# Performance work log

Hardware: AMD Instinct MI355X
Metric: run time of the kernel (lower is better)

Reference implementation:

```python
import jax, jax.numpy as jnp
import numpy as np

B, D, U1, U2 = 16384, 512, 512, 512
BN_EPS = 1e-3  # keras BatchNormalization default epsilon


def sparsemax(z):
    # z: [..., D]; standard sparsemax along last axis (Martins & Astudillo)
    d = z.shape[-1]
    z_sorted = -jnp.sort(-z, axis=-1)                      # descending
    z_cum = jnp.cumsum(z_sorted, axis=-1)
    k = jnp.arange(1, d + 1, dtype=z.dtype)
    support = (1.0 + k * z_sorted) > z_cum                 # [..., D] bool
    k_z = jnp.sum(support, axis=-1, keepdims=True)         # support size
    tau = (jnp.take_along_axis(z_cum, k_z.astype(jnp.int32) - 1, axis=-1) - 1.0) / k_z.astype(z.dtype)
    return jnp.maximum(z - tau, 0.0)


def setup_inputs() -> dict:
    key = jax.random.key(0)
    ks = jax.random.split(key, 8)
    x = jax.random.normal(ks[0], (B, D), dtype=jnp.float32)
    W1 = jax.random.normal(ks[1], (D, U1), dtype=jnp.float32) * 0.05
    b1 = jnp.zeros((U1,), jnp.float32)
    centers = jax.random.normal(ks[2], (U2, D), dtype=jnp.float32)      # paraboloid centers
    coefs = jax.random.normal(ks[3], (U2, D), dtype=jnp.float32) * 0.1  # paraboloid axis coefficients
    bn_gamma = jnp.ones((D,), jnp.float32)
    bn_beta = jnp.zeros((D,), jnp.float32)
    bn_mean = jnp.zeros((D,), jnp.float32)
    bn_var = jnp.ones((D,), jnp.float32)
    W_out = jax.random.normal(ks[4], (U1 + U2, D), dtype=jnp.float32) * 0.05
    b_out = jnp.zeros((D,), jnp.float32)
    w_add = jnp.array([0.5, 0.5], jnp.float32)  # WeightedAdd learnable scalars
    return {"x": x, "W1": W1, "b1": b1, "centers": centers, "coefs": coefs,
            "bn_gamma": bn_gamma, "bn_beta": bn_beta, "bn_mean": bn_mean, "bn_var": bn_var,
            "W_out": W_out, "b_out": b_out, "w_add": w_add}


def reference(x, W1, b1, centers, coefs, bn_gamma, bn_beta, bn_mean, bn_var, W_out, b_out, w_add):
    # Dense branch
    h1 = jax.nn.relu(x @ W1 + b1)                               # [B, U1]
    # BoundedParaboloids branch: BatchNorm (inference stats) then bounded paraboloids
    xb = (x - bn_mean) * jax.lax.rsqrt(bn_var + BN_EPS) * bn_gamma + bn_beta
    # q_j = sum_d (coefs[j,d] * (xb_d - centers[j,d]))^2, computed via GEMMs
    A = coefs * coefs                                            # [U2, D]
    q = (xb * xb) @ A.T - 2.0 * (xb @ (A * centers).T) + jnp.sum(A * centers * centers, axis=-1)
    h2 = jax.nn.relu(1.0 - q)                                    # [B, U2] bounded paraboloids
    # Output embedding: Dense(relu) on concat
    emb = jax.nn.relu(jnp.concatenate([h1, h2], axis=-1) @ W_out + b_out)  # [B, D]
    # WeightedAdd of (dropout-identity) inputs and embedding; dropout_rate=0 / inference
    pre = w_add[0] * x + w_add[1] * emb
    mask = sparsemax(pre)                                        # [B, D]
    return mask
```

## Files before the change

kernel.cpp:

```cpp
#include <hip/hip_runtime.h>
#include <math.h>

typedef float f4 __attribute__((ext_vector_type(4)));
typedef float f32x4 __attribute__((ext_vector_type(4)));
typedef __bf16 bf16x8 __attribute__((ext_vector_type(8)));
typedef unsigned short u16;
typedef u16 us8 __attribute__((ext_vector_type(8)));

__device__ __forceinline__ u16 f2bf(float f) {
  unsigned u = __builtin_bit_cast(unsigned, f);
  unsigned r = u + 0x7fffu + ((u >> 16) & 1u);
  return (u16)(r >> 16);
}
__device__ __forceinline__ float bf2f(u16 h) {
  unsigned u = ((unsigned)h) << 16;
  return __builtin_bit_cast(float, u);
}

__global__ __launch_bounds__(256) void prep_bn_kernel(
    const float* __restrict__ gamma, const float* __restrict__ beta,
    const float* __restrict__ mean, const float* __restrict__ var,
    float* __restrict__ scale, float* __restrict__ shift) {
  int d = blockIdx.x * blockDim.x + threadIdx.x;
  if (d < 512) {
    float s = rsqrtf(var[d] + 1e-3f) * gamma[d];
    scale[d] = s;
    shift[d] = beta[d] - mean[d] * s;
  }
}

__global__ __launch_bounds__(64) void prep_params_kernel(
    const float* __restrict__ coefs, const float* __restrict__ centers,
    u16* __restrict__ pth, float* __restrict__ cvec) {
  int j = blockIdx.x;
  int l = threadIdx.x;
  int d0 = l * 8;
  f4 c0 = *(const f4*)(coefs + (size_t)j * 512 + d0);
  f4 c1 = *(const f4*)(coefs + (size_t)j * 512 + d0 + 4);
  f4 e0 = *(const f4*)(centers + (size_t)j * 512 + d0);
  f4 e1 = *(const f4*)(centers + (size_t)j * 512 + d0 + 4);
  us8 pa, pb;
  float acc = 0.f;
#pragma unroll
  for (int e = 0; e < 8; ++e) {
    float cf = (e < 4) ? c0[e] : c1[e - 4];
    float ce = (e < 4) ? e0[e] : e1[e - 4];
    float a = cf * cf;
    pa[e] = f2bf(a);
    pb[e] = f2bf(-2.f * a * ce);
    acc = fmaf(a * ce, ce, acc);
  }
  *(us8*)(pth + (size_t)j * 1024 + d0) = pa;
  *(us8*)(pth + (size_t)j * 1024 + 512 + d0) = pb;
#pragma unroll
  for (int off = 32; off; off >>= 1) acc += __shfl_xor(acc, off);
  if (l == 0) cvec[j] = acc;
}

__global__ __launch_bounds__(256) void transpose_split_kernel(
    const float* __restrict__ in, u16* __restrict__ th, int K, int N) {
  __shared__ float t[32][33];
  int lx = threadIdx.x;
  int ly = threadIdx.y;
  int n0 = blockIdx.x * 32, k0 = blockIdx.y * 32;
#pragma unroll
  for (int i = 0; i < 4; ++i)
    t[ly + 8 * i][lx] = in[(size_t)(k0 + ly + 8 * i) * N + n0 + lx];
  __syncthreads();
#pragma unroll
  for (int i = 0; i < 4; ++i) {
    float v = t[lx][ly + 8 * i];
    th[(size_t)(n0 + ly + 8 * i) * K + k0 + lx] = f2bf(v);
  }
}

__global__ __launch_bounds__(256) void conv_x_kernel(
    const float* __restrict__ x, const float* __restrict__ scale,
    const float* __restrict__ shift, u16* __restrict__ xh,
    u16* __restrict__ xb, u16* __restrict__ xsq) {
  int gid = blockIdx.x * 256 + threadIdx.x;
  int m = gid >> 6;
  int d0 = (gid & 63) * 8;
  f4 v0 = *(const f4*)(x + (size_t)m * 512 + d0);
  f4 v1 = *(const f4*)(x + (size_t)m * 512 + d0 + 4);
  f4 s0 = *(const f4*)(scale + d0);
  f4 s1 = *(const f4*)(scale + d0 + 4);
  f4 h0 = *(const f4*)(shift + d0);
  f4 h1 = *(const f4*)(shift + d0 + 4);
  us8 oh, ob, oq;
#pragma unroll
  for (int e = 0; e < 8; ++e) {
    float xv = (e < 4) ? v0[e] : v1[e - 4];
    float sc = (e < 4) ? s0[e] : s1[e - 4];
    float sh = (e < 4) ? h0[e] : h1[e - 4];
    oh[e] = f2bf(xv);
    float xbf = fmaf(xv, sc, sh);
    ob[e] = f2bf(xbf);
    oq[e] = f2bf(xbf * xbf);
  }
  *(us8*)(xh + (size_t)m * 512 + d0) = oh;
  *(us8*)(xb + (size_t)m * 512 + d0) = ob;
  *(us8*)(xsq + (size_t)m * 512 + d0) = oq;
}

__device__ __forceinline__ void wait_vm8() {
  asm volatile("s_waitcnt vmcnt(8)" ::: "memory");
}
__device__ __forceinline__ void wait_vm0() {
  asm volatile("s_waitcnt vmcnt(0)" ::: "memory");
}
__device__ __forceinline__ void sbar() { __builtin_amdgcn_s_barrier(); }
__device__ __forceinline__ void sgb0() { __builtin_amdgcn_sched_barrier(0); }

__global__ __launch_bounds__(256, 2) void gemm_fused12(
    const u16* __restrict__ Xh, const u16* __restrict__ Xb,
    const u16* __restrict__ Xsq, const u16* __restrict__ W1th,
    const u16* __restrict__ Pth, const float* __restrict__ b1,
    const float* __restrict__ cvec, u16* __restrict__ Hout) {
  extern __shared__ char smem[];
  const int tid = threadIdx.x;
  const int l = tid & 63;
  const int w = tid >> 6;
  const int wm = w & 1, wn = w >> 1;
  const int lr = l & 15, lk = l >> 4;
  const int sx = lr & 7;
  const int bid = blockIdx.x;
  const int L = (bid & 7) * 128 + (bid >> 3);
  const int p = L >> 3;
  const int g = ((L >> 2) & 1) ^ 1;
  const int n = L & 3;
  const int m0 = p * 128, n0 = n * 128;
  const int Kg = g ? 1024 : 512;
  const int nt = g ? 16 : 8;
  const u16* Bmat = g ? Pth : W1th;
  const int srow = l >> 3;
  const int sslot = (l & 7) ^ srow;

  f32x4 acc[4][4];
#pragma unroll
  for (int i = 0; i < 4; ++i)
#pragma unroll
    for (int j = 0; j < 4; ++j) acc[i][j] = (f32x4){0.f, 0.f, 0.f, 0.f};

#define F12_STAGE(buf, k0)                                                    \
  {                                                                           \
    const u16* Asrc = g ? (((k0) < 512) ? Xsq : Xb) : Xh;                     \
    const int kb = (k0)&511;                                                  \
    char* dA = smem + (buf)*16384;                                            \
    char* dB = smem + 32768 + (buf)*16384;                                    \
    _Pragma("unroll") for (int pp = 0; pp < 4; ++pp) {                        \
      int c = pp * 4 + w;                                                     \
      int row = c * 8 + srow;                                                 \
      int loff = c * 1024;                                                    \
      size_t goa = (size_t)(m0 + row) * 512 + kb + sslot * 8;                 \
      size_t gob = (size_t)(n0 + row) * Kg + (k0) + sslot * 8;                \
      __builtin_amdgcn_global_load_lds(                                       \
          (const __attribute__((address_space(1))) void*)(Asrc + goa),        \
          (__attribute__((address_space(3))) void*)(dA + loff), 16, 0, 0);    \
      __builtin_amdgcn_global_load_lds(                                       \
          (const __attribute__((address_space(1))) void*)(Bmat + gob),        \
          (__attribute__((address_space(3))) void*)(dB + loff), 16, 0, 0);    \
    }                                                                         \
  }

  F12_STAGE(0, 0);
  F12_STAGE(1, 64);
  for (int t = 0; t < nt; ++t) {
    if (t + 1 < nt) {
      wait_vm8();
    } else {
      wait_vm0();
    }
    sgb0();
    sbar();
    sgb0();
    const char* sA = smem + (t & 1) * 16384;
    const char* sB = smem + 32768 + (t & 1) * 16384;
#pragma unroll
    for (int ks = 0; ks < 2; ++ks) {
      bf16x8 av[4], bv[4];
#pragma unroll
      for (int i = 0; i < 4; ++i)
        av[i] = *(const bf16x8*)(sA + (wm * 64 + i * 16 + lr) * 128 +
                                 (((ks * 4 + lk) ^ sx) * 16));
#pragma unroll
      for (int j = 0; j < 4; ++j)
        bv[j] = *(const bf16x8*)(sB + (wn * 64 + j * 16 + lr) * 128 +
                                 (((ks * 4 + lk) ^ sx) * 16));
#pragma unroll
      for (int i = 0; i < 4; ++i)
#pragma unroll
        for (int j = 0; j < 4; ++j)
          acc[i][j] = __builtin_amdgcn_mfma_f32_16x16x32_bf16(av[i], bv[j],
                                                              acc[i][j], 0, 0, 0);
    }
    sgb0();
    sbar();
    sgb0();
    if (t + 2 < nt) F12_STAGE(t & 1, (t + 2) * 64);
  }
#undef F12_STAGE

  const int mwb = m0 + wm * 64;
  const int nwb = n0 + wn * 64;
  const float* bias = g ? cvec : b1;
#pragma unroll
  for (int j = 0; j < 4; ++j) {
    int nn = nwb + j * 16 + lr;
    float bv = bias[nn];
#pragma unroll
    for (int i = 0; i < 4; ++i) {
#pragma unroll
      for (int r = 0; r < 4; ++r) {
        int m = mwb + i * 16 + lk * 4 + r;
        float v = acc[i][j][r] + bv;
        v = g ? fmaxf(1.f - v, 0.f) : fmaxf(v, 0.f);
        Hout[(size_t)m * 1024 + g * 512 + nn] = f2bf(v);
      }
    }
  }
}

__global__ __launch_bounds__(256, 2) void gemm3(
    const u16* __restrict__ Ah, const u16* __restrict__ Bh,
    const float* __restrict__ bias, const float* __restrict__ xorig,
    const float* __restrict__ wadd, u16* __restrict__ preb) {
  extern __shared__ char smem[];
  const int tid = threadIdx.x;
  const int l = tid & 63;
  const int w = tid >> 6;
  const int wm = w & 1, wn = w >> 1;
  const int lr = l & 15, lk = l >> 4;
  const int sx = lr & 7;
  const int bid = blockIdx.x;
  const int lin = (bid & 7) * 64 + (bid >> 3);
  const int m0 = (lin >> 2) * 128, n0 = (lin & 3) * 128;
  const int srow = l >> 3;
  const int sslot = (l & 7) ^ srow;

  f32x4 acc[4][4];
#pragma unroll
  for (int i = 0; i < 4; ++i)
#pragma unroll
    for (int j = 0; j < 4; ++j) acc[i][j] = (f32x4){0.f, 0.f, 0.f, 0.f};

#define G3_STAGE(buf, k0)                                                     \
  {                                                                           \
    char* dA = smem + (buf)*16384;                                            \
    char* dB = smem + 32768 + (buf)*16384;                                    \
    _Pragma("unroll") for (int pp = 0; pp < 4; ++pp) {                        \
      int c = pp * 4 + w;                                                     \
      int row = c * 8 + srow;                                                 \
      int loff = c * 1024;                                                    \
      size_t gob = (size_t)(n0 + row) * 1024 + (k0) + sslot * 8;              \
      size_t goa = (size_t)(m0 + row) * 1024 + (k0) + sslot * 8;              \
      __builtin_amdgcn_global_load_lds(                                       \
          (const __attribute__((address_space(1))) void*)(Bh + gob),          \
          (__attribute__((address_space(3))) void*)(dB + loff), 16, 0, 0);    \
      __builtin_amdgcn_global_load_lds(                                       \
          (const __attribute__((address_space(1))) void*)(Ah + goa),          \
          (__attribute__((address_space(3))) void*)(dA + loff), 16, 0, 0);    \
    }                                                                         \
  }

  G3_STAGE(0, 0);
  G3_STAGE(1, 64);
  for (int t = 0; t < 16; ++t) {
    if (t + 1 < 16) {
      wait_vm8();
    } else {
      wait_vm0();
    }
    sgb0();
    sbar();
    sgb0();
    const char* sA = smem + (t & 1) * 16384;
    const char* sB = smem + 32768 + (t & 1) * 16384;
#pragma unroll
    for (int ks = 0; ks < 2; ++ks) {
      bf16x8 av[4], bv[4];
#pragma unroll
      for (int i = 0; i < 4; ++i)
        av[i] = *(const bf16x8*)(sA + (wm * 64 + i * 16 + lr) * 128 +
                                 (((ks * 4 + lk) ^ sx) * 16));
#pragma unroll
      for (int j = 0; j < 4; ++j)
        bv[j] = *(const bf16x8*)(sB + (wn * 64 + j * 16 + lr) * 128 +
                                 (((ks * 4 + lk) ^ sx) * 16));
#pragma unroll
      for (int i = 0; i < 4; ++i)
#pragma unroll
        for (int j = 0; j < 4; ++j)
          acc[i][j] = __builtin_amdgcn_mfma_f32_16x16x32_bf16(av[i], bv[j],
                                                              acc[i][j], 0, 0, 0);
    }
    sgb0();
    sbar();
    sgb0();
    if (t + 2 < 16) G3_STAGE(t & 1, (t + 2) * 64);
  }
#undef G3_STAGE

  const int mwb = m0 + wm * 64;
  const int nwb = n0 + wn * 64;
  float w0 = wadd[0], w1 = wadd[1];
#pragma unroll
  for (int j = 0; j < 4; ++j) {
    int n = nwb + j * 16 + lr;
    float bv = bias[n];
#pragma unroll
    for (int i = 0; i < 4; ++i) {
#pragma unroll
      for (int r = 0; r < 4; ++r) {
        int m = mwb + i * 16 + lk * 4 + r;
        float v = fmaxf(acc[i][j][r] + bv, 0.f);
        preb[(size_t)m * 512 + n] =
            f2bf(fmaf(w1, v, w0 * xorig[(size_t)m * 512 + n]));
      }
    }
  }
}

__global__ __launch_bounds__(256) void sparsemax_kernel(
    const u16* __restrict__ pre, float* __restrict__ out) {
  int wrk = (blockIdx.x & 7) * 512 + (blockIdx.x >> 3);
  int row = wrk * 4 + (threadIdx.x >> 6);
  int lane = threadIdx.x & 63;
  const u16* rp = pre + (size_t)row * 512;
  us8 zv = *(const us8*)(rp + lane * 8);
  float z[8];
#pragma unroll
  for (int e = 0; e < 8; ++e) z[e] = bf2f(zv[e]);
  float m = z[0];
#pragma unroll
  for (int i = 1; i < 8; ++i) m = fmaxf(m, z[i]);
#pragma unroll
  for (int off = 32; off; off >>= 1) m = fmaxf(m, __shfl_xor(m, off));
  float tau = m - 1.0f;
  for (int it = 0; it < 32; ++it) {
    float s = 0.f, k = 0.f;
#pragma unroll
    for (int i = 0; i < 8; ++i) {
      if (z[i] > tau) {
        s += z[i] - tau;
        k += 1.f;
      }
    }
#pragma unroll
    for (int off = 32; off; off >>= 1) {
      s += __shfl_xor(s, off);
      k += __shfl_xor(k, off);
    }
    if (k < 0.5f) break;
    float tn = tau + (s - 1.f) / k;
    if (tn == tau) break;
    tau = tn;
  }
  float s = 0.f, k = 0.f;
#pragma unroll
  for (int i = 0; i < 8; ++i)
    if (z[i] > tau) {
      s += z[i];
      k += 1.f;
    }
#pragma unroll
  for (int off = 32; off; off >>= 1) {
    s += __shfl_xor(s, off);
    k += __shfl_xor(k, off);
  }
  float tauf = (k >= 0.5f) ? (s - 1.f) / k : (m - 1.f);
  float* op = out + (size_t)row * 512 + lane * 8;
  f4 o0, o1;
#pragma unroll
  for (int e = 0; e < 4; ++e) {
    o0[e] = fmaxf(z[e] - tauf, 0.f);
    o1[e] = fmaxf(z[4 + e] - tauf, 0.f);
  }
  *(f4*)(op) = o0;
  *(f4*)(op + 4) = o1;
}

extern "C" void kernel_launch(void* const* d_in, const int* in_sizes, int n_in,
                              void* d_out, int out_size, void* d_ws,
                              size_t ws_size, hipStream_t stream) {
  const float* x = (const float*)d_in[0];
  const float* W1 = (const float*)d_in[1];
  const float* b1 = (const float*)d_in[2];
  const float* centers = (const float*)d_in[3];
  const float* coefs = (const float*)d_in[4];
  const float* gamma = (const float*)d_in[5];
  const float* beta = (const float*)d_in[6];
  const float* mean = (const float*)d_in[7];
  const float* var = (const float*)d_in[8];
  const float* W_out = (const float*)d_in[9];
  const float* b_out = (const float*)d_in[10];
  const float* wadd = (const float*)d_in[11];
  float* out = (float*)d_out;

  char* ws = (char*)d_ws;
  u16* Hh = (u16*)(ws);
  u16* Xh = (u16*)(ws + 33554432);
  u16* Xb = (u16*)(ws + 50331648);
  char* pool = ws + 67108864;
  u16* W1th = (u16*)(pool);
  u16* Pth = (u16*)(pool + 1048576);
  float* cvec = (float*)(ws + 69206016);
  float* scale = (float*)(ws + 69208064);
  float* shift = (float*)(ws + 69210112);
  u16* Xsq = (u16*)d_out;
  u16* preb = Xb;
  const bool bigws = (ws_size >= (size_t)70260736);
  u16* Wth = bigws ? (u16*)(ws + 69212160) : (u16*)(pool);

  prep_bn_kernel<<<2, 256, 0, stream>>>(gamma, beta, mean, var, scale, shift);
  prep_params_kernel<<<512, 64, 0, stream>>>(coefs, centers, Pth, cvec);
  transpose_split_kernel<<<dim3(16, 16), dim3(32, 8), 0, stream>>>(W1, W1th,
                                                                   512, 512);
  if (bigws) {
    transpose_split_kernel<<<dim3(16, 32), dim3(32, 8), 0, stream>>>(
        W_out, Wth, 1024, 512);
  }
  conv_x_kernel<<<4096, 256, 0, stream>>>(x, scale, shift, Xh, Xb, Xsq);

  gemm_fused12<<<1024, 256, 65536, stream>>>(Xh, Xb, Xsq, W1th, Pth, b1, cvec,
                                             Hh);

  if (!bigws) {
    transpose_split_kernel<<<dim3(16, 32), dim3(32, 8), 0, stream>>>(
        W_out, Wth, 1024, 512);
  }
  gemm3<<<512, 256, 65536, stream>>>(Hh, Wth, b_out, x, wadd, preb);
  sparsemax_kernel<<<4096, 256, 0, stream>>>(preb, out);
}
```

Baseline: 104.3 us.

## Fold batchnorm into W1 so the dense GEMM reuses normalized x

Rewrites x@W1 as xb@(W1/scale) with an adjusted bias b1 - (shift/scale)@W1, computed by a new small reduction kernel. This removes the separate bf16 copy of raw x (one 16MB write and its reads in the GEMM), so both GEMM branches read the same normalized input. It risks a numerical difference when the BN scale is tiny (division by scale) and adds an extra small kernel launch. The workspace layout is also reorganized and the W_out transpose now always runs early.

```diff
diff --git a/kernel.cpp b/kernel.cpp
--- a/kernel.cpp
+++ b/kernel.cpp
@@ -58,7 +58,8 @@
 }
 
 __global__ __launch_bounds__(256) void transpose_split_kernel(
-    const float* __restrict__ in, u16* __restrict__ th, int K, int N) {
+    const float* __restrict__ in, u16* __restrict__ th,
+    const float* __restrict__ scale, int K, int N) {
   __shared__ float t[32][33];
   int lx = threadIdx.x;
   int ly = threadIdx.y;
@@ -67,17 +68,41 @@
   for (int i = 0; i < 4; ++i)
     t[ly + 8 * i][lx] = in[(size_t)(k0 + ly + 8 * i) * N + n0 + lx];
   __syncthreads();
+  float rs = scale ? (1.0f / scale[k0 + lx]) : 1.0f;
 #pragma unroll
   for (int i = 0; i < 4; ++i) {
-    float v = t[lx][ly + 8 * i];
+    float v = t[lx][ly + 8 * i] * rs;
     th[(size_t)(n0 + ly + 8 * i) * K + k0 + lx] = f2bf(v);
+  }
+}
+
+__global__ __launch_bounds__(256) void b1adj_kernel(
+    const float* __restrict__ W1, const float* __restrict__ b1,
+    const float* __restrict__ scale, const float* __restrict__ shift,
+    float* __restrict__ b1a) {
+  __shared__ float red[4][64];
+  int b = blockIdx.x;
+  int lane = threadIdx.x & 63;
+  int kq = threadIdx.x >> 6;
+  int j = b * 64 + lane;
+  float partial = 0.f;
+  for (int i = 0; i < 128; ++i) {
+    int k = kq * 128 + i;
+    partial = fmaf(shift[k] / scale[k], W1[(size_t)k * 512 + j], partial);
+  }
+  red[kq][lane] = partial;
+  __syncthreads();
+  if (threadIdx.x < 64) {
+    float t = red[0][threadIdx.x] + red[1][threadIdx.x] +
+              red[2][threadIdx.x] + red[3][threadIdx.x];
+    b1a[b * 64 + threadIdx.x] = b1[b * 64 + threadIdx.x] - t;
   }
 }
 
 __global__ __launch_bounds__(256) void conv_x_kernel(
     const float* __restrict__ x, const float* __restrict__ scale,
-    const float* __restrict__ shift, u16* __restrict__ xh,
-    u16* __restrict__ xb, u16* __restrict__ xsq) {
+    const float* __restrict__ shift, u16* __restrict__ xb,
+    u16* __restrict__ xsq) {
   int gid = blockIdx.x * 256 + threadIdx.x;
   int m = gid >> 6;
   int d0 = (gid & 63) * 8;
@@ -87,18 +112,16 @@
   f4 s1 = *(const f4*)(scale + d0 + 4);
   f4 h0 = *(const f4*)(shift + d0);
   f4 h1 = *(const f4*)(shift + d0 + 4);
-  us8 oh, ob, oq;
+  us8 ob, oq;
 #pragma unroll
   for (int e = 0; e < 8; ++e) {
     float xv = (e < 4) ? v0[e] : v1[e - 4];
     float sc = (e < 4) ? s0[e] : s1[e - 4];
     float sh = (e < 4) ? h0[e] : h1[e - 4];
-    oh[e] = f2bf(xv);
     float xbf = fmaf(xv, sc, sh);
     ob[e] = f2bf(xbf);
     oq[e] = f2bf(xbf * xbf);
   }
-  *(us8*)(xh + (size_t)m * 512 + d0) = oh;
   *(us8*)(xb + (size_t)m * 512 + d0) = ob;
   *(us8*)(xsq + (size_t)m * 512 + d0) = oq;
 }
@@ -113,10 +136,10 @@
 __device__ __forceinline__ void sgb0() { __builtin_amdgcn_sched_barrier(0); }
 
 __global__ __launch_bounds__(256, 2) void gemm_fused12(
-    const u16* __restrict__ Xh, const u16* __restrict__ Xb,
-    const u16* __restrict__ Xsq, const u16* __restrict__ W1th,
-    const u16* __restrict__ Pth, const float* __restrict__ b1,
-    const float* __restrict__ cvec, u16* __restrict__ Hout) {
+    const u16* __restrict__ Xb, const u16* __restrict__ Xsq,
+    const u16* __restrict__ W1th, const u16* __restrict__ Pth,
+    const float* __restrict__ b1a, const float* __restrict__ cvec,
+    u16* __restrict__ Hout) {
   extern __shared__ char smem[];
   const int tid = threadIdx.x;
   const int l = tid & 63;
@@ -144,7 +167,7 @@
 
 #define F12_STAGE(buf, k0)                                                    \
   {                                                                           \
-    const u16* Asrc = g ? (((k0) < 512) ? Xsq : Xb) : Xh;                     \
+    const u16* Asrc = g ? (((k0) < 512) ? Xsq : Xb) : Xb;                     \
     const int kb = (k0)&511;                                                  \
     char* dA = smem + (buf)*16384;                                            \
     char* dB = smem + 32768 + (buf)*16384;                                    \
@@ -203,7 +226,7 @@
 
   const int mwb = m0 + wm * 64;
   const int nwb = n0 + wn * 64;
-  const float* bias = g ? cvec : b1;
+  const float* bias = g ? cvec : b1a;
 #pragma unroll
   for (int j = 0; j < 4; ++j) {
     int nn = nwb + j * 16 + lr;
@@ -399,36 +422,28 @@
 
   char* ws = (char*)d_ws;
   u16* Hh = (u16*)(ws);
-  u16* Xh = (u16*)(ws + 33554432);
+  float* b1a = (float*)(ws + 33554432);
+  u16* Wth = (u16*)(ws + 33562624);
   u16* Xb = (u16*)(ws + 50331648);
-  char* pool = ws + 67108864;
-  u16* W1th = (u16*)(pool);
-  u16* Pth = (u16*)(pool + 1048576);
+  u16* Pth = (u16*)(ws + 67108864);
+  u16* W1th = (u16*)(ws + 68157440);
   float* cvec = (float*)(ws + 69206016);
   float* scale = (float*)(ws + 69208064);
   float* shift = (float*)(ws + 69210112);
   u16* Xsq = (u16*)d_out;
   u16* preb = Xb;
-  const bool bigws = (ws_size >= (size_t)70260736);
-  u16* Wth = bigws ? (u16*)(ws + 69212160) : (u16*)(pool);
 
   prep_bn_kernel<<<2, 256, 0, stream>>>(gamma, beta, mean, var, scale, shift);
   prep_params_kernel<<<512, 64, 0, stream>>>(coefs, centers, Pth, cvec);
-  transpose_split_kernel<<<dim3(16, 16), dim3(32, 8), 0, stream>>>(W1, W1th,
-                                                                   512, 512);
-  if (bigws) {
-    transpose_split_kernel<<<dim3(16, 32), dim3(32, 8), 0, stream>>>(
-        W_out, Wth, 1024, 512);
-  }
-  conv_x_kernel<<<4096, 256, 0, stream>>>(x, scale, shift, Xh, Xb, Xsq);
-
-  gemm_fused12<<<1024, 256, 65536, stream>>>(Xh, Xb, Xsq, W1th, Pth, b1, cvec,
+  transpose_split_kernel<<<dim3(16, 16), dim3(32, 8), 0, stream>>>(
+      W1, W1th, scale, 512, 512);
+  b1adj_kernel<<<8, 256, 0, stream>>>(W1, b1, scale, shift, b1a);
+  transpose_split_kernel<<<dim3(16, 32), dim3(32, 8), 0, stream>>>(
+      W_out, Wth, nullptr, 1024, 512);
+  conv_x_kernel<<<4096, 256, 0, stream>>>(x, scale, shift, Xb, Xsq);
+
+  gemm_fused12<<<1024, 256, 65536, stream>>>(Xb, Xsq, W1th, Pth, b1a, cvec,
                                              Hh);
-
-  if (!bigws) {
-    transpose_split_kernel<<<dim3(16, 32), dim3(32, 8), 0, stream>>>(
-        W_out, Wth, 1024, 512);
-  }
   gemm3<<<512, 256, 65536, stream>>>(Hh, Wth, b_out, x, wadd, preb);
   sparsemax_kernel<<<4096, 256, 0, stream>>>(preb, out);
 }
```

New measurement: 113.9 us. +9.2%, slower.
